# Kernel optimization log

Hardware: AMD Instinct MI355X
Metric: run time of the kernel (lower is better)

Reference implementation:

```python
import jax, jax.numpy as jnp
import numpy as np

B, S, H = 4, 2048, 2048      # batch, seq, hidden_size
E, K, F = 8, 2, 1408         # n_routed_experts, topk, moe_inter_dim


def setup_inputs() -> dict:
    key = jax.random.key(0)
    k0, k1, k2, k3, k4 = jax.random.split(key, 5)
    s = 0.02  # init scale for weights
    return {
        "hidden_states": jax.random.normal(k0, (B, S, H), dtype=jnp.float32),
        "router_w": jax.random.normal(k1, (E, H), dtype=jnp.float32) * s,
        "gate_w": jax.random.normal(k2, (E, F, H), dtype=jnp.float32) * s,
        "up_w": jax.random.normal(k3, (E, F, H), dtype=jnp.float32) * s,
        "down_w": jax.random.normal(k4, (E, H, F), dtype=jnp.float32) * s,
    }


def reference(hidden_states, router_w, gate_w, up_w, down_w):
    shape = hidden_states.shape
    x = hidden_states.reshape(-1, H)                  # [T, H], T = B*S
    # Router: softmax over all experts, then top-k of the probabilities
    logits = x @ router_w.T                            # [T, E]
    weights = jax.nn.softmax(logits, axis=-1)          # [T, E]
    topk_weight, indices = jax.lax.top_k(weights, K)   # [T, K]
    # normalize_top_k_affinities
    topk_weight = topk_weight / (topk_weight.sum(axis=-1, keepdims=True) + 1e-20)
    # Per-token per-expert combine weight: [T, E]
    combine = jnp.einsum("tk,tke->te", topk_weight,
                         jax.nn.one_hot(indices, E, dtype=topk_weight.dtype))
    # Experts: swiglu MLP, weighted-combined. Loop over the small fixed set of experts.
    out = jnp.zeros_like(x)
    for e in range(E):
        h = jax.nn.silu(x @ gate_w[e].T) * (x @ up_w[e].T)  # [T, F]
        out = out + combine[:, e:e + 1] * (h @ down_w[e].T)  # [T, H]
    return out.reshape(shape)
```

## Files before the change

### kernel.cpp

```cpp
#include <hip/hip_runtime.h>
#include <stdint.h>

#define T_TOK 8192
#define HD 2048
#define NE 8
#define FD 1408
#define BM 256
#define BN1 128
#define BN2 128
#define BK 64
#define MAXT 72
#define ROWS_CAP 18432

typedef unsigned short u16;
typedef __attribute__((ext_vector_type(8))) short bf16x8;
typedef __attribute__((ext_vector_type(4))) float f32x4;

__device__ __forceinline__ u16 f2bf(float f) {
  unsigned u = __float_as_uint(f);
  unsigned r = (u + 0x7fffu + ((u >> 16) & 1u)) >> 16;
  return (u16)r;
}
__device__ __forceinline__ float bflo(unsigned u) { return __uint_as_float(u << 16); }
__device__ __forceinline__ float bfhi(unsigned u) { return __uint_as_float(u & 0xffff0000u); }

__device__ __forceinline__ void async_copy16(const void* g, void* l) {
  __builtin_amdgcn_global_load_lds(
      (__attribute__((address_space(1))) void*)(uintptr_t)g,
      (__attribute__((address_space(3))) void*)(uintptr_t)l,
      16, 0, 0);
}

__device__ __forceinline__ void conv4(const float* __restrict__ s, u16* __restrict__ d, long j) {
  float4 v = ((const float4*)s)[j];
  ushort4 o;
  o.x = f2bf(v.x); o.y = f2bf(v.y); o.z = f2bf(v.z); o.w = f2bf(v.w);
  ((ushort4*)d)[j] = o;
}

__global__ __launch_bounds__(256) void k_router(
    const float* __restrict__ x, const float* __restrict__ rw,
    const float* __restrict__ gw, const float* __restrict__ uw, const float* __restrict__ dw,
    u16* __restrict__ xb, u16* __restrict__ gwb, u16* __restrict__ uwb, u16* __restrict__ dwb,
    int* __restrict__ topk_idx, float* __restrict__ topk_w)
{
  int t = blockIdx.x;
  int tid = threadIdx.x;
  int lane = tid & 63;
  int wave = tid >> 6;
  const float4* xr = (const float4*)(x + (size_t)t * HD);
  const float4* w0 = (const float4*)(rw + (size_t)(wave * 2) * HD);
  const float4* w1 = (const float4*)(rw + (size_t)(wave * 2 + 1) * HD);
  float a0 = 0.f, a1 = 0.f;
  for (int i = lane; i < HD / 4; i += 64) {
    float4 xv = xr[i], v0 = w0[i], v1 = w1[i];
    a0 += xv.x * v0.x + xv.y * v0.y + xv.z * v0.z + xv.w * v0.w;
    a1 += xv.x * v1.x + xv.y * v1.y + xv.z * v1.z + xv.w * v1.w;
  }
  {
    float4 v0 = xr[tid * 2], v1 = xr[tid * 2 + 1];
    uint4 o;
    o.x = (unsigned)f2bf(v0.x) | ((unsigned)f2bf(v0.y) << 16);
    o.y = (unsigned)f2bf(v0.z) | ((unsigned)f2bf(v0.w) << 16);
    o.z = (unsigned)f2bf(v1.x) | ((unsigned)f2bf(v1.y) << 16);
    o.w = (unsigned)f2bf(v1.z) | ((unsigned)f2bf(v1.w) << 16);
    ((uint4*)(xb + (size_t)t * HD))[tid] = o;
  }
#pragma unroll
  for (int off = 32; off > 0; off >>= 1) {
    a0 += __shfl_down(a0, off);
    a1 += __shfl_down(a1, off);
  }
  __shared__ float lg[NE];
  if (lane == 0) { lg[wave * 2] = a0; lg[wave * 2 + 1] = a1; }
  __syncthreads();
  if (tid == 0) {
    float m1 = lg[0], m2 = -3.4e38f;
    int i1 = 0, i2 = 0;
    for (int e = 1; e < NE; e++) {
      float v = lg[e];
      if (v > m1)      { m2 = m1; i2 = i1; m1 = v; i1 = e; }
      else if (v > m2) { m2 = v; i2 = e; }
    }
    float wA = 1.f / (1.f + expf(m2 - m1));
    float wB = 1.f - wA;
    topk_idx[t * 2] = i1; topk_idx[t * 2 + 1] = i2;
    topk_w[t * 2] = wA;   topk_w[t * 2 + 1] = wB;
  }
  const long n_w = (long)NE * FD * HD / 4;
  const long gstride = (long)gridDim.x * 256;
  const long g0 = (long)t * 256 + tid;
  for (long j = g0; j < n_w; j += gstride) conv4(gw, gwb, j);
  for (long j = g0; j < n_w; j += gstride) conv4(uw, uwb, j);
  for (long j = g0; j < n_w; j += gstride) conv4(dw, dwb, j);
}

__global__ __launch_bounds__(256) void k_meta_scatter(
    const int* __restrict__ topk_idx, int* __restrict__ meta,
    int* __restrict__ row_token, int* __restrict__ tokrow)
{
  __shared__ int scan[NE][257];
  __shared__ int roff[NE], tstart[NE + 1];
  int tid = threadIdx.x;
  for (int i = tid; i < ROWS_CAP; i += 256) row_token[i] = 0;
  if (tid < NE) scan[tid][0] = 0;
  int cnt[NE] = {};
  int base_i = tid * 64;
#pragma unroll 4
  for (int j = 0; j < 64; j++) {
    int v = topk_idx[base_i + j];
#pragma unroll
    for (int e = 0; e < NE; e++) cnt[e] += (v == e);
  }
  int i = tid + 1;
#pragma unroll
  for (int e = 0; e < NE; e++) scan[e][i] = cnt[e];
  __syncthreads();
  for (int s = 1; s < 256; s <<= 1) {
    int add[NE];
#pragma unroll
    for (int e = 0; e < NE; e++) add[e] = (i >= s) ? scan[e][i - s] : 0;
    __syncthreads();
#pragma unroll
    for (int e = 0; e < NE; e++) scan[e][i] += add[e];
    __syncthreads();
  }
  if (tid == 0) {
    int off = 0, nt = 0;
    for (int e = 0; e < NE; e++) {
      int tot = scan[e][256];
      int tiles = (tot + BM - 1) / BM;
      roff[e] = off;
      tstart[e] = nt;
      nt += tiles;
      off += tiles * BM;
    }
    tstart[NE] = nt;
    meta[8] = nt;
  }
  __syncthreads();
  int nt = tstart[NE];
  if (tid < nt) {
    int e = 0;
#pragma unroll
    for (int k = 1; k < NE; k++) e += (tid >= tstart[k]);
    meta[64 + tid] = e;
    meta[256 + tid] = roff[e] + (tid - tstart[e]) * BM;
  }
  int pos[NE];
#pragma unroll
  for (int e = 0; e < NE; e++) pos[e] = roff[e] + scan[e][tid];
  for (int j = 0; j < 64; j++) {
    int idx = base_i + j;
    int v = topk_idx[idx];
    int p = 0;
#pragma unroll
    for (int e = 0; e < NE; e++) if (v == e) p = pos[e]++;
    row_token[p] = idx >> 1;
    tokrow[idx] = p;
  }
}

__global__ __launch_bounds__(512, 2) void k_gemm1(
    const u16* __restrict__ xb, const u16* __restrict__ gwb, const u16* __restrict__ uwb,
    const int* __restrict__ meta, const int* __restrict__ row_token, u16* __restrict__ hb)
{
  int total = meta[8];
  int mt = (int)blockIdx.x;
  mt = (mt & 7) * 9 + (mt >> 3);
  if (mt >= total) return;
  int e = meta[64 + mt];
  int row0 = meta[256 + mt];
  int ntile = blockIdx.y;

  __shared__ u16 As[2][BM * BK];
  __shared__ u16 Bg[2][BN1 * BK];
  __shared__ u16 Bu[2][BN1 * BK];

  int lane = threadIdx.x & 63;
  int wave = threadIdx.x >> 6;
  int wr = wave >> 1, wc = wave & 1;

  const u16* aG[4]; unsigned aOff[4];
  const u16* gG[2]; const u16* uG[2]; unsigned bOff[2];
#pragma unroll
  for (int j = 0; j < 4; j++) {
    int r = wave * 32 + j * 8 + (lane >> 3);
    int c = (lane & 7) ^ (r & 7);
    int tok = row_token[row0 + r];
    aG[j] = xb + (size_t)tok * HD + c * 8;
    aOff[j] = (unsigned)(wave * 32 + j * 8) * 128;
  }
#pragma unroll
  for (int j = 0; j < 2; j++) {
    int r = wave * 16 + j * 8 + (lane >> 3);
    int c = (lane & 7) ^ (r & 7);
    int nrow = ntile * BN1 + r;
    size_t wof = ((size_t)e * FD + nrow) * HD + c * 8;
    gG[j] = gwb + wof;
    uG[j] = uwb + wof;
    bOff[j] = (unsigned)(wave * 16 + j * 8) * 128;
  }

  f32x4 accG[4][4] = {};
  f32x4 accU[4][4] = {};

#pragma unroll
  for (int j = 0; j < 4; j++) async_copy16(aG[j], (char*)As[0] + aOff[j]);
#pragma unroll
  for (int j = 0; j < 2; j++) async_copy16(gG[j], (char*)Bg[0] + bOff[j]);
#pragma unroll
  for (int j = 0; j < 2; j++) async_copy16(uG[j], (char*)Bu[0] + bOff[j]);
  asm volatile("s_waitcnt vmcnt(0)" ::: "memory");
  __builtin_amdgcn_sched_barrier(0);
  __builtin_amdgcn_s_barrier();

  int cur = 0;
  for (int kt = 0; kt < HD / BK; kt++) {
    if (kt + 1 < HD / BK) {
      int ko = (kt + 1) * BK;
#pragma unroll
      for (int j = 0; j < 4; j++) async_copy16(aG[j] + ko, (char*)As[cur ^ 1] + aOff[j]);
#pragma unroll
      for (int j = 0; j < 2; j++) async_copy16(gG[j] + ko, (char*)Bg[cur ^ 1] + bOff[j]);
#pragma unroll
      for (int j = 0; j < 2; j++) async_copy16(uG[j] + ko, (char*)Bu[cur ^ 1] + bOff[j]);
    }
#pragma unroll
    for (int kk = 0; kk < 2; kk++) {
      bf16x8 av[4], gv[4], uv[4];
#pragma unroll
      for (int mi = 0; mi < 4; mi++) {
        int r = wr * 64 + mi * 16 + (lane & 15);
        int slot = (kk * 4 + (lane >> 4)) ^ (r & 7);
        av[mi] = *(const bf16x8*)((const char*)As[cur] + (unsigned)(r * 8 + slot) * 16);
      }
#pragma unroll
      for (int ni = 0; ni < 4; ni++) {
        int r = wc * 64 + ni * 16 + (lane & 15);
        int slot = (kk * 4 + (lane >> 4)) ^ (r & 7);
        gv[ni] = *(const bf16x8*)((const char*)Bg[cur] + (unsigned)(r * 8 + slot) * 16);
        uv[ni] = *(const bf16x8*)((const char*)Bu[cur] + (unsigned)(r * 8 + slot) * 16);
      }
      __builtin_amdgcn_s_setprio(1);
#pragma unroll
      for (int mi = 0; mi < 4; mi++)
#pragma unroll
        for (int ni = 0; ni < 4; ni++) {
          accG[mi][ni] = __builtin_amdgcn_mfma_f32_16x16x32_bf16(av[mi], gv[ni], accG[mi][ni], 0, 0, 0);
          accU[mi][ni] = __builtin_amdgcn_mfma_f32_16x16x32_bf16(av[mi], uv[ni], accU[mi][ni], 0, 0, 0);
        }
      __builtin_amdgcn_s_setprio(0);
    }
    asm volatile("s_waitcnt vmcnt(0)" ::: "memory");
    __builtin_amdgcn_sched_barrier(0);
    __builtin_amdgcn_s_barrier();
    cur ^= 1;
  }

#pragma unroll
  for (int mi = 0; mi < 4; mi++) {
#pragma unroll
    for (int r = 0; r < 4; r++) {
      int row = row0 + wr * 64 + mi * 16 + (lane >> 4) * 4 + r;
      u16* hrow = hb + (size_t)row * FD + ntile * BN1 + wc * 64 + (lane & 15);
#pragma unroll
      for (int ni = 0; ni < 4; ni++) {
        float g = accG[mi][ni][r];
        float u = accU[mi][ni][r];
        float s = g / (1.f + __expf(-g));
        hrow[ni * 16] = f2bf(s * u);
      }
    }
  }
}

__global__ __launch_bounds__(512, 2) void k_gemm2(
    const u16* __restrict__ hb, const u16* __restrict__ dwb,
    const int* __restrict__ meta, u16* __restrict__ Y)
{
  int total = meta[8];
  int mt = (int)blockIdx.x;
  mt = (mt & 7) * 9 + (mt >> 3);
  if (mt >= total) return;
  int e = meta[64 + mt];
  int row0 = meta[256 + mt];
  int ntile = blockIdx.y;

  __shared__ u16 As[2][BM * BK];
  __shared__ u16 Bs[2][BN2 * BK];

  int lane = threadIdx.x & 63;
  int wave = threadIdx.x >> 6;
  int wr = wave >> 1, wc = wave & 1;

  const u16* aG[4]; unsigned aOff[4];
  const u16* bG[2]; unsigned bOff[2];
#pragma unroll
  for (int j = 0; j < 4; j++) {
    int r = wave * 32 + j * 8 + (lane >> 3);
    int c = (lane & 7) ^ (r & 7);
    aG[j] = hb + (size_t)(row0 + r) * FD + c * 8;
    aOff[j] = (unsigned)(wave * 32 + j * 8) * 128;
  }
#pragma unroll
  for (int j = 0; j < 2; j++) {
    int r = wave * 16 + j * 8 + (lane >> 3);
    int c = (lane & 7) ^ (r & 7);
    int nrow = ntile * BN2 + r;
    bG[j] = dwb + ((size_t)e * HD + nrow) * FD + c * 8;
    bOff[j] = (unsigned)(wave * 16 + j * 8) * 128;
  }

  f32x4 acc[4][4] = {};

#pragma unroll
  for (int j = 0; j < 4; j++) async_copy16(aG[j], (char*)As[0] + aOff[j]);
#pragma unroll
  for (int j = 0; j < 2; j++) async_copy16(bG[j], (char*)Bs[0] + bOff[j]);
  asm volatile("s_waitcnt vmcnt(0)" ::: "memory");
  __builtin_amdgcn_sched_barrier(0);
  __builtin_amdgcn_s_barrier();

  int cur = 0;
  for (int kt = 0; kt < FD / BK; kt++) {
    if (kt + 1 < FD / BK) {
      int ko = (kt + 1) * BK;
#pragma unroll
      for (int j = 0; j < 4; j++) async_copy16(aG[j] + ko, (char*)As[cur ^ 1] + aOff[j]);
#pragma unroll
      for (int j = 0; j < 2; j++) async_copy16(bG[j] + ko, (char*)Bs[cur ^ 1] + bOff[j]);
    }
#pragma unroll
    for (int kk = 0; kk < 2; kk++) {
      bf16x8 av[4], bv[4];
#pragma unroll
      for (int mi = 0; mi < 4; mi++) {
        int r = wr * 64 + mi * 16 + (lane & 15);
        int slot = (kk * 4 + (lane >> 4)) ^ (r & 7);
        av[mi] = *(const bf16x8*)((const char*)As[cur] + (unsigned)(r * 8 + slot) * 16);
      }
#pragma unroll
      for (int ni = 0; ni < 4; ni++) {
        int r = wc * 64 + ni * 16 + (lane & 15);
        int slot = (kk * 4 + (lane >> 4)) ^ (r & 7);
        bv[ni] = *(const bf16x8*)((const char*)Bs[cur] + (unsigned)(r * 8 + slot) * 16);
      }
      __builtin_amdgcn_s_setprio(1);
#pragma unroll
      for (int mi = 0; mi < 4; mi++)
#pragma unroll
        for (int ni = 0; ni < 4; ni++)
          acc[mi][ni] = __builtin_amdgcn_mfma_f32_16x16x32_bf16(av[mi], bv[ni], acc[mi][ni], 0, 0, 0);
      __builtin_amdgcn_s_setprio(0);
    }
    asm volatile("s_waitcnt vmcnt(0)" ::: "memory");
    __builtin_amdgcn_sched_barrier(0);
    __builtin_amdgcn_s_barrier();
    cur ^= 1;
  }

#pragma unroll
  for (int mi = 0; mi < 4; mi++) {
#pragma unroll
    for (int r = 0; r < 4; r++) {
      int grow = row0 + wr * 64 + mi * 16 + (lane >> 4) * 4 + r;
      u16* yrow = Y + (size_t)grow * HD + ntile * BN2 + wc * 64 + (lane & 15);
#pragma unroll
      for (int ni = 0; ni < 4; ni++)
        yrow[ni * 16] = f2bf(acc[mi][ni][r]);
    }
  }
}

__global__ __launch_bounds__(256) void k_combine(
    const u16* __restrict__ Y, const int* __restrict__ tokrow,
    const float* __restrict__ topk_w, float* __restrict__ out)
{
  int t = blockIdx.x;
  int i = threadIdx.x;
  int rA = tokrow[t * 2], rB = tokrow[t * 2 + 1];
  float wA = topk_w[t * 2], wB = topk_w[t * 2 + 1];
  uint4 a = *(const uint4*)(Y + (size_t)rA * HD + i * 8);
  uint4 b = *(const uint4*)(Y + (size_t)rB * HD + i * 8);
  float4 o0, o1;
  o0.x = wA * bflo(a.x) + wB * bflo(b.x);
  o0.y = wA * bfhi(a.x) + wB * bfhi(b.x);
  o0.z = wA * bflo(a.y) + wB * bflo(b.y);
  o0.w = wA * bfhi(a.y) + wB * bfhi(b.y);
  o1.x = wA * bflo(a.z) + wB * bflo(b.z);
  o1.y = wA * bfhi(a.z) + wB * bfhi(b.z);
  o1.z = wA * bflo(a.w) + wB * bflo(b.w);
  o1.w = wA * bfhi(a.w) + wB * bfhi(b.w);
  float* op = out + (size_t)t * HD + i * 8;
  *(float4*)op = o0;
  *(float4*)(op + 4) = o1;
}

extern "C" void kernel_launch(void* const* d_in, const int* in_sizes, int n_in,
                              void* d_out, int out_size, void* d_ws, size_t ws_size,
                              hipStream_t stream) {
  const float* x  = (const float*)d_in[0];
  const float* rw = (const float*)d_in[1];
  const float* gw = (const float*)d_in[2];
  const float* uw = (const float*)d_in[3];
  const float* dw = (const float*)d_in[4];
  float* out = (float*)d_out;

  char* w = (char*)d_ws;
  int*   meta      = (int*)w;
  int*   row_token = (int*)(w + 4096);
  int*   topk_idx  = (int*)(w + 4096 + ROWS_CAP * 4);
  float* topk_w    = (float*)(w + 4096 + ROWS_CAP * 4 + T_TOK * 2 * 4);
  int*   tokrow    = (int*)(w + 4096 + ROWS_CAP * 4 + T_TOK * 4 * 4);
  size_t off = (size_t)1 << 20;
  u16* xb  = (u16*)(w + off); off += (size_t)T_TOK * HD * 2;
  u16* gwb = (u16*)(w + off); off += (size_t)NE * FD * HD * 2;
  u16* uwb = (u16*)(w + off); off += (size_t)NE * FD * HD * 2;
  u16* dwb = (u16*)(w + off); off += (size_t)NE * HD * FD * 2;
  u16* hb  = (u16*)(w + off);
  u16* Y = xb;

  k_router<<<T_TOK, 256, 0, stream>>>(x, rw, gw, uw, dw, xb, gwb, uwb, dwb, topk_idx, topk_w);
  k_meta_scatter<<<1, 256, 0, stream>>>(topk_idx, meta, row_token, tokrow);
  k_gemm1<<<dim3(MAXT, FD / BN1), 512, 0, stream>>>(xb, gwb, uwb, meta, row_token, hb);
  k_gemm2<<<dim3(MAXT, HD / BN2), 512, 0, stream>>>(hb, dwb, meta, Y);
  k_combine<<<T_TOK, 256, 0, stream>>>(Y, tokrow, topk_w, out);
}
```

Before: 747.7 us.

## Widen grouped GEMM tiles to 256x256 with interleaved gate/up rows and XCD-aware grid

Both expert GEMMs move to 256x256 output tiles over 8 waves in a 2x4 layout, with 32 accumulators per wave. In gemm1 the gate and up weight rows are interleaved in 16-row groups inside one B tile, so one MFMA stream produces both projections and SwiGLU is applied from adjacent accumulators. The grid is flattened so that blocks sharing an expert tile stay on the same XCD. The pipeline now waits only on the previous stage (vmcnt(8)) before the barrier, which allows more load/compute overlap. The cost is higher register pressure from the larger accumulator set and fewer blocks in the grid.

```diff
diff --git a/kernel.cpp b/kernel.cpp
--- a/kernel.cpp
+++ b/kernel.cpp
@@ -6,10 +6,7 @@
 #define NE 8
 #define FD 1408
 #define BM 256
-#define BN1 128
-#define BN2 128
 #define BK 64
-#define MAXT 72
 #define ROWS_CAP 18432
 
 typedef unsigned short u16;
@@ -166,111 +163,99 @@
     const int* __restrict__ meta, const int* __restrict__ row_token, u16* __restrict__ hb)
 {
   int total = meta[8];
-  int mt = (int)blockIdx.x;
-  mt = (mt & 7) * 9 + (mt >> 3);
+  int b = (int)blockIdx.x;
+  int xcd = b & 7, s = b >> 3;
+  int ntile = s / 9;
+  int mt = xcd * 9 + (s % 9);
   if (mt >= total) return;
   int e = meta[64 + mt];
   int row0 = meta[256 + mt];
-  int ntile = blockIdx.y;
 
   __shared__ u16 As[2][BM * BK];
-  __shared__ u16 Bg[2][BN1 * BK];
-  __shared__ u16 Bu[2][BN1 * BK];
-
-  int lane = threadIdx.x & 63;
-  int wave = threadIdx.x >> 6;
-  int wr = wave >> 1, wc = wave & 1;
-
-  const u16* aG[4]; unsigned aOff[4];
-  const u16* gG[2]; const u16* uG[2]; unsigned bOff[2];
+  __shared__ u16 Bs[2][BM * BK];
+
+  int tid = threadIdx.x;
+  int lane = tid & 63;
+  int wave = tid >> 6;
+  int wr = wave >> 2, wc = wave & 3;
+
+  const u16* aSrc[4]; const u16* bSrc[4];
+  unsigned ldsOff[4];
 #pragma unroll
   for (int j = 0; j < 4; j++) {
-    int r = wave * 32 + j * 8 + (lane >> 3);
-    int c = (lane & 7) ^ (r & 7);
+    int g = j * 512 + tid;
+    int r = g >> 3, slot = g & 7;
+    int col = (slot ^ (r & 7)) * 8;
     int tok = row_token[row0 + r];
-    aG[j] = xb + (size_t)tok * HD + c * 8;
-    aOff[j] = (unsigned)(wave * 32 + j * 8) * 128;
-  }
-#pragma unroll
-  for (int j = 0; j < 2; j++) {
-    int r = wave * 16 + j * 8 + (lane >> 3);
-    int c = (lane & 7) ^ (r & 7);
-    int nrow = ntile * BN1 + r;
-    size_t wof = ((size_t)e * FD + nrow) * HD + c * 8;
-    gG[j] = gwb + wof;
-    uG[j] = uwb + wof;
-    bOff[j] = (unsigned)(wave * 16 + j * 8) * 128;
-  }
-
-  f32x4 accG[4][4] = {};
-  f32x4 accU[4][4] = {};
-
-#pragma unroll
-  for (int j = 0; j < 4; j++) async_copy16(aG[j], (char*)As[0] + aOff[j]);
-#pragma unroll
-  for (int j = 0; j < 2; j++) async_copy16(gG[j], (char*)Bg[0] + bOff[j]);
-#pragma unroll
-  for (int j = 0; j < 2; j++) async_copy16(uG[j], (char*)Bu[0] + bOff[j]);
-  asm volatile("s_waitcnt vmcnt(0)" ::: "memory");
-  __builtin_amdgcn_sched_barrier(0);
-  __builtin_amdgcn_s_barrier();
-
-  int cur = 0;
-  for (int kt = 0; kt < HD / BK; kt++) {
-    if (kt + 1 < HD / BK) {
+    aSrc[j] = xb + (size_t)tok * HD + col;
+    int type = (r >> 4) & 1;
+    int frow = (r >> 5) * 16 + (r & 15);
+    const u16* wbase = type ? uwb : gwb;
+    bSrc[j] = wbase + ((size_t)e * FD + ntile * 128 + frow) * HD + col;
+    ldsOff[j] = (unsigned)(j * 512 + wave * 64) * 16;
+  }
+
+  f32x4 acc[8][4] = {};
+
+#pragma unroll
+  for (int j = 0; j < 4; j++) async_copy16(aSrc[j], (char*)As[0] + ldsOff[j]);
+#pragma unroll
+  for (int j = 0; j < 4; j++) async_copy16(bSrc[j], (char*)Bs[0] + ldsOff[j]);
+
+  const int NK = HD / BK;
+  for (int kt = 0; kt < NK; kt++) {
+    int cur = kt & 1;
+    if (kt + 1 < NK) {
       int ko = (kt + 1) * BK;
 #pragma unroll
-      for (int j = 0; j < 4; j++) async_copy16(aG[j] + ko, (char*)As[cur ^ 1] + aOff[j]);
-#pragma unroll
-      for (int j = 0; j < 2; j++) async_copy16(gG[j] + ko, (char*)Bg[cur ^ 1] + bOff[j]);
-#pragma unroll
-      for (int j = 0; j < 2; j++) async_copy16(uG[j] + ko, (char*)Bu[cur ^ 1] + bOff[j]);
-    }
+      for (int j = 0; j < 4; j++) async_copy16(aSrc[j] + ko, (char*)As[cur ^ 1] + ldsOff[j]);
+#pragma unroll
+      for (int j = 0; j < 4; j++) async_copy16(bSrc[j] + ko, (char*)Bs[cur ^ 1] + ldsOff[j]);
+      asm volatile("s_waitcnt vmcnt(8)" ::: "memory");
+    } else {
+      asm volatile("s_waitcnt vmcnt(0)" ::: "memory");
+    }
+    __builtin_amdgcn_sched_barrier(0);
+    __builtin_amdgcn_s_barrier();
+    asm volatile("" ::: "memory");
 #pragma unroll
     for (int kk = 0; kk < 2; kk++) {
-      bf16x8 av[4], gv[4], uv[4];
-#pragma unroll
-      for (int mi = 0; mi < 4; mi++) {
-        int r = wr * 64 + mi * 16 + (lane & 15);
+      bf16x8 av[8], bv[4];
+#pragma unroll
+      for (int mi = 0; mi < 8; mi++) {
+        int r = wr * 128 + mi * 16 + (lane & 15);
         int slot = (kk * 4 + (lane >> 4)) ^ (r & 7);
         av[mi] = *(const bf16x8*)((const char*)As[cur] + (unsigned)(r * 8 + slot) * 16);
       }
 #pragma unroll
       for (int ni = 0; ni < 4; ni++) {
-        int r = wc * 64 + ni * 16 + (lane & 15);
-        int slot = (kk * 4 + (lane >> 4)) ^ (r & 7);
-        gv[ni] = *(const bf16x8*)((const char*)Bg[cur] + (unsigned)(r * 8 + slot) * 16);
-        uv[ni] = *(const bf16x8*)((const char*)Bu[cur] + (unsigned)(r * 8 + slot) * 16);
+        int p = wc * 64 + ni * 16 + (lane & 15);
+        int slot = (kk * 4 + (lane >> 4)) ^ (p & 7);
+        bv[ni] = *(const bf16x8*)((const char*)Bs[cur] + (unsigned)(p * 8 + slot) * 16);
       }
       __builtin_amdgcn_s_setprio(1);
 #pragma unroll
-      for (int mi = 0; mi < 4; mi++)
-#pragma unroll
-        for (int ni = 0; ni < 4; ni++) {
-          accG[mi][ni] = __builtin_amdgcn_mfma_f32_16x16x32_bf16(av[mi], gv[ni], accG[mi][ni], 0, 0, 0);
-          accU[mi][ni] = __builtin_amdgcn_mfma_f32_16x16x32_bf16(av[mi], uv[ni], accU[mi][ni], 0, 0, 0);
-        }
+      for (int mi = 0; mi < 8; mi++)
+#pragma unroll
+        for (int ni = 0; ni < 4; ni++)
+          acc[mi][ni] = __builtin_amdgcn_mfma_f32_16x16x32_bf16(av[mi], bv[ni], acc[mi][ni], 0, 0, 0);
       __builtin_amdgcn_s_setprio(0);
     }
-    asm volatile("s_waitcnt vmcnt(0)" ::: "memory");
-    __builtin_amdgcn_sched_barrier(0);
+    asm volatile("" ::: "memory");
     __builtin_amdgcn_s_barrier();
-    cur ^= 1;
-  }
-
-#pragma unroll
-  for (int mi = 0; mi < 4; mi++) {
-#pragma unroll
-    for (int r = 0; r < 4; r++) {
-      int row = row0 + wr * 64 + mi * 16 + (lane >> 4) * 4 + r;
-      u16* hrow = hb + (size_t)row * FD + ntile * BN1 + wc * 64 + (lane & 15);
-#pragma unroll
-      for (int ni = 0; ni < 4; ni++) {
-        float g = accG[mi][ni][r];
-        float u = accU[mi][ni][r];
-        float s = g / (1.f + __expf(-g));
-        hrow[ni * 16] = f2bf(s * u);
-      }
+    asm volatile("" ::: "memory");
+  }
+
+#pragma unroll
+  for (int mi = 0; mi < 8; mi++) {
+#pragma unroll
+    for (int rr = 0; rr < 4; rr++) {
+      int row = row0 + wr * 128 + mi * 16 + (lane >> 4) * 4 + rr;
+      u16* hrow = hb + (size_t)row * FD + ntile * 128 + wc * 32 + (lane & 15);
+      float g0 = acc[mi][0][rr], u0 = acc[mi][1][rr];
+      hrow[0]  = f2bf(u0 * (g0 / (1.f + __expf(-g0))));
+      float g1 = acc[mi][2][rr], u1 = acc[mi][3][rr];
+      hrow[16] = f2bf(u1 * (g1 / (1.f + __expf(-g1))));
     }
   }
 }
@@ -280,95 +265,95 @@
     const int* __restrict__ meta, u16* __restrict__ Y)
 {
   int total = meta[8];
-  int mt = (int)blockIdx.x;
-  mt = (mt & 7) * 9 + (mt >> 3);
+  int b = (int)blockIdx.x;
+  int xcd = b & 7, s = b >> 3;
+  int ntile = s / 9;
+  int mt = xcd * 9 + (s % 9);
   if (mt >= total) return;
   int e = meta[64 + mt];
   int row0 = meta[256 + mt];
-  int ntile = blockIdx.y;
 
   __shared__ u16 As[2][BM * BK];
-  __shared__ u16 Bs[2][BN2 * BK];
-
-  int lane = threadIdx.x & 63;
-  int wave = threadIdx.x >> 6;
-  int wr = wave >> 1, wc = wave & 1;
-
-  const u16* aG[4]; unsigned aOff[4];
-  const u16* bG[2]; unsigned bOff[2];
+  __shared__ u16 Bs[2][BM * BK];
+
+  int tid = threadIdx.x;
+  int lane = tid & 63;
+  int wave = tid >> 6;
+  int wr = wave >> 2, wc = wave & 3;
+
+  const u16* aSrc[4]; const u16* bSrc[4];
+  unsigned ldsOff[4];
 #pragma unroll
   for (int j = 0; j < 4; j++) {
-    int r = wave * 32 + j * 8 + (lane >> 3);
-    int c = (lane & 7) ^ (r & 7);
-    aG[j] = hb + (size_t)(row0 + r) * FD + c * 8;
-    aOff[j] = (unsigned)(wave * 32 + j * 8) * 128;
-  }
-#pragma unroll
-  for (int j = 0; j < 2; j++) {
-    int r = wave * 16 + j * 8 + (lane >> 3);
-    int c = (lane & 7) ^ (r & 7);
-    int nrow = ntile * BN2 + r;
-    bG[j] = dwb + ((size_t)e * HD + nrow) * FD + c * 8;
-    bOff[j] = (unsigned)(wave * 16 + j * 8) * 128;
-  }
-
-  f32x4 acc[4][4] = {};
-
-#pragma unroll
-  for (int j = 0; j < 4; j++) async_copy16(aG[j], (char*)As[0] + aOff[j]);
-#pragma unroll
-  for (int j = 0; j < 2; j++) async_copy16(bG[j], (char*)Bs[0] + bOff[j]);
-  asm volatile("s_waitcnt vmcnt(0)" ::: "memory");
-  __builtin_amdgcn_sched_barrier(0);
-  __builtin_amdgcn_s_barrier();
-
-  int cur = 0;
-  for (int kt = 0; kt < FD / BK; kt++) {
-    if (kt + 1 < FD / BK) {
+    int g = j * 512 + tid;
+    int r = g >> 3, slot = g & 7;
+    int col = (slot ^ (r & 7)) * 8;
+    aSrc[j] = hb + (size_t)(row0 + r) * FD + col;
+    int nrow = ntile * 256 + r;
+    bSrc[j] = dwb + ((size_t)e * HD + nrow) * FD + col;
+    ldsOff[j] = (unsigned)(j * 512 + wave * 64) * 16;
+  }
+
+  f32x4 acc[8][4] = {};
+
+#pragma unroll
+  for (int j = 0; j < 4; j++) async_copy16(aSrc[j], (char*)As[0] + ldsOff[j]);
+#pragma unroll
+  for (int j = 0; j < 4; j++) async_copy16(bSrc[j], (char*)Bs[0] + ldsOff[j]);
+
+  const int NK = FD / BK;
+  for (int kt = 0; kt < NK; kt++) {
+    int cur = kt & 1;
+    if (kt + 1 < NK) {
       int ko = (kt + 1) * BK;
 #pragma unroll
-      for (int j = 0; j < 4; j++) async_copy16(aG[j] + ko, (char*)As[cur ^ 1] + aOff[j]);
-#pragma unroll
-      for (int j = 0; j < 2; j++) async_copy16(bG[j] + ko, (char*)Bs[cur ^ 1] + bOff[j]);
-    }
+      for (int j = 0; j < 4; j++) async_copy16(aSrc[j] + ko, (char*)As[cur ^ 1] + ldsOff[j]);
+#pragma unroll
+      for (int j = 0; j < 4; j++) async_copy16(bSrc[j] + ko, (char*)Bs[cur ^ 1] + ldsOff[j]);
+      asm volatile("s_waitcnt vmcnt(8)" ::: "memory");
+    } else {
+      asm volatile("s_waitcnt vmcnt(0)" ::: "memory");
+    }
+    __builtin_amdgcn_sched_barrier(0);
+    __builtin_amdgcn_s_barrier();
+    asm volatile("" ::: "memory");
 #pragma unroll
     for (int kk = 0; kk < 2; kk++) {
-      bf16x8 av[4], bv[4];
-#pragma unroll
-      for (int mi = 0; mi < 4; mi++) {
-        int r = wr * 64 + mi * 16 + (lane & 15);
+      bf16x8 av[8], bv[4];
+#pragma unroll
+      for (int mi = 0; mi < 8; mi++) {
+        int r = wr * 128 + mi * 16 + (lane & 15);
         int slot = (kk * 4 + (lane >> 4)) ^ (r & 7);
         av[mi] = *(const bf16x8*)((const char*)As[cur] + (unsigned)(r * 8 + slot) * 16);
       }
 #pragma unroll
       for (int ni = 0; ni < 4; ni++) {
-        int r = wc * 64 + ni * 16 + (lane & 15);
-        int slot = (kk * 4 + (lane >> 4)) ^ (r & 7);
-        bv[ni] = *(const bf16x8*)((const char*)Bs[cur] + (unsigned)(r * 8 + slot) * 16);
+        int p = wc * 64 + ni * 16 + (lane & 15);
+        int slot = (kk * 4 + (lane >> 4)) ^ (p & 7);
+        bv[ni] = *(const bf16x8*)((const char*)Bs[cur] + (unsigned)(p * 8 + slot) * 16);
       }
       __builtin_amdgcn_s_setprio(1);
 #pragma unroll
-      for (int mi = 0; mi < 4; mi++)
+      for (int mi = 0; mi < 8; mi++)
 #pragma unroll
         for (int ni = 0; ni < 4; ni++)
           acc[mi][ni] = __builtin_amdgcn_mfma_f32_16x16x32_bf16(av[mi], bv[ni], acc[mi][ni], 0, 0, 0);
       __builtin_amdgcn_s_setprio(0);
     }
-    asm volatile("s_waitcnt vmcnt(0)" ::: "memory");
-    __builtin_amdgcn_sched_barrier(0);
+    asm volatile("" ::: "memory");
     __builtin_amdgcn_s_barrier();
-    cur ^= 1;
-  }
-
-#pragma unroll
-  for (int mi = 0; mi < 4; mi++) {
-#pragma unroll
-    for (int r = 0; r < 4; r++) {
-      int grow = row0 + wr * 64 + mi * 16 + (lane >> 4) * 4 + r;
-      u16* yrow = Y + (size_t)grow * HD + ntile * BN2 + wc * 64 + (lane & 15);
+    asm volatile("" ::: "memory");
+  }
+
+#pragma unroll
+  for (int mi = 0; mi < 8; mi++) {
+#pragma unroll
+    for (int rr = 0; rr < 4; rr++) {
+      int grow = row0 + wr * 128 + mi * 16 + (lane >> 4) * 4 + rr;
+      u16* yrow = Y + (size_t)grow * HD + ntile * 256 + wc * 64 + (lane & 15);
 #pragma unroll
       for (int ni = 0; ni < 4; ni++)
-        yrow[ni * 16] = f2bf(acc[mi][ni][r]);
+        yrow[ni * 16] = f2bf(acc[mi][ni][rr]);
     }
   }
 }
@@ -423,7 +408,7 @@
 
   k_router<<<T_TOK, 256, 0, stream>>>(x, rw, gw, uw, dw, xb, gwb, uwb, dwb, topk_idx, topk_w);
   k_meta_scatter<<<1, 256, 0, stream>>>(topk_idx, meta, row_token, tokrow);
-  k_gemm1<<<dim3(MAXT, FD / BN1), 512, 0, stream>>>(xb, gwb, uwb, meta, row_token, hb);
-  k_gemm2<<<dim3(MAXT, HD / BN2), 512, 0, stream>>>(hb, dwb, meta, Y);
+  k_gemm1<<<8 * 11 * 9, 512, 0, stream>>>(xb, gwb, uwb, meta, row_token, hb);
+  k_gemm2<<<8 * 8 * 9, 512, 0, stream>>>(hb, dwb, meta, Y);
   k_combine<<<T_TOK, 256, 0, stream>>>(Y, tokrow, topk_w, out);
 }
```

New measurement: 771.6 us. +3.2%, slower.
